# Kernel tuning notes

Hardware: AMD Instinct MI355X
Metric: run time of the kernel (lower is better)

Reference implementation:

```python
import jax, jax.numpy as jnp
import numpy as np


def lstm_encode(x, Wih, Whh, b):
    """x: [S, T, F] -> final hidden state [S, H]. PyTorch LSTM gate order (i, f, g, o)."""
    S = x.shape[0]
    H = Whh.shape[1]

    def step(carry, xt):
        h, c = carry
        z = xt @ Wih.T + h @ Whh.T + b  # [S, 4H]
        i, f, g, o = jnp.split(z, 4, axis=-1)
        c = jax.nn.sigmoid(f) * c + jax.nn.sigmoid(i) * jnp.tanh(g)
        h = jax.nn.sigmoid(o) * jnp.tanh(c)
        return (h, c), None

    init = (jnp.zeros((S, H), x.dtype), jnp.zeros((S, H), x.dtype))
    (h, _), _ = jax.lax.scan(step, init, jnp.swapaxes(x, 0, 1))
    return h


def gatv2(h, Ws, Wd, a, bias):
    """Dense GATv2 on batched fully-connected graphs (no self loops).
    h: [G, N, Hin]; Ws, Wd: [nh, Hin, O]; a: [nh, O]; bias: [nh, O] -> [G, N, nh, O].
    Graph is fully connected (all i != j), so edge-softmax == dense row softmax
    with the diagonal masked out; this is the efficient dense form of the
    gather / LeakyReLU / edge-softmax / scatter pattern in DGL's GATv2Conv."""
    nh = Ws.shape[0]
    N = h.shape[1]
    self_mask = jnp.eye(N, dtype=bool)
    outs = []
    for hd in range(nh):  # small fixed head count; loop caps peak memory
        fs = h @ Ws[hd]  # [G, N, O] source-projected feats (messages)
        fd = h @ Wd[hd]  # [G, N, O] dst-projected feats
        e = jax.nn.leaky_relu(fd[:, :, None, :] + fs[:, None, :, :], 0.2)  # [G, dst, src, O]
        logits = jnp.where(self_mask, -jnp.inf, e @ a[hd])  # [G, dst, src]
        attn = jax.nn.softmax(logits, axis=-1)
        outs.append(jnp.einsum('gds,gso->gdo', attn, fs) + bias[hd])
    return jnp.stack(outs, axis=2)


def cosine(x, y, eps=1e-6):
    xn = x / jnp.maximum(jnp.linalg.norm(x, axis=-1, keepdims=True), eps)
    yn = y / jnp.maximum(jnp.linalg.norm(y, axis=-1, keepdims=True), eps)
    return (xn * yn).sum(-1)


def setup_inputs() -> dict:
    key = jax.random.key(0)
    B, K, T, N, F, H, GH, NH = 16, 4, 64, 128, 16, 32, 32, 8
    ks = jax.random.split(key, 16)

    def rn(k, shape, scale=1.0):
        return jax.random.normal(k, shape, jnp.float32) * scale

    return {
        'anchor': rn(ks[0], (B, T, N, F)),
        'pos': rn(ks[1], (B, T, N, F)),
        'neg': rn(ks[2], (B, K, T, N, F)),
        'hideout': rn(ks[3], (B, 2)),
        'timestep': jax.random.uniform(ks[4], (B, 1), jnp.float32),
        'Wih': rn(ks[5], (4 * H, F), 1.0 / np.sqrt(F)),
        'Whh': rn(ks[6], (4 * H, H), 1.0 / np.sqrt(H)),
        'b_lstm': rn(ks[7], (4 * H,), 0.1),
        'W1s': rn(ks[8], (NH, H, H), 1.0 / np.sqrt(H)),
        'W1d': rn(ks[9], (NH, H, H), 1.0 / np.sqrt(H)),
        'a1': rn(ks[10], (NH, H), 1.0 / np.sqrt(H)),
        'b1': rn(ks[11], (NH, H), 0.1),
        'W2s': rn(ks[12], (1, H, GH), 1.0 / np.sqrt(H)),
        'W2d': rn(ks[13], (1, H, GH), 1.0 / np.sqrt(H)),
        'a2': rn(ks[14], (1, GH), 1.0 / np.sqrt(GH)),
        'b2': rn(ks[15], (1, GH), 0.1),
        'num_agents': 128,
    }


def reference(anchor, pos, neg, hideout, timestep, Wih, Whh, b_lstm,
              W1s, W1d, a1, b1, W2s, W2d, a2, b2, num_agents):
    B, T, N, F = anchor.shape
    K = neg.shape[1]
    H = Whh.shape[1]
    # per-agent time series -> LSTM sequences
    a_seq = jnp.transpose(anchor, (0, 2, 1, 3)).reshape(B * N, T, F)
    p_seq = jnp.transpose(pos, (0, 2, 1, 3)).reshape(B * N, T, F)
    n_seq = jnp.transpose(neg, (0, 1, 3, 2, 4)).reshape(B * K * N, T, F)
    hn = lstm_encode(jnp.concatenate([a_seq, p_seq, n_seq], 0), Wih, Whh, b_lstm)
    hg = hn.reshape(-1, N, H)  # [(2+K)*B, N, H] batched fully-connected graphs
    h1 = gatv2(hg, W1s, W1d, a1, b1).mean(axis=2)  # mean over 8 heads
    h2 = gatv2(h1, W2s, W2d, a2, b2)[:, :, 0, :]   # single head, squeezed
    pooled = h2.mean(axis=1)                        # AvgPooling over nodes
    anchor_res = pooled[:B]
    pos_res = pooled[B:2 * B]
    neg_res = pooled[2 * B:].reshape(B, K, -1)
    sim_pos = cosine(anchor_res, pos_res)[:, None]      # [B, 1]
    sim_neg = cosine(anchor_res[:, None, :], neg_res)   # [B, K]
    all_vecs = jnp.concatenate([sim_neg, sim_pos], axis=1)  # positive last
    contrastive = (-jax.nn.log_softmax(all_vecs, axis=1)[:, -1]).mean()
    res = jnp.concatenate([anchor_res, hideout, timestep], axis=-1)
    return res, contrastive
```

## Files before the change

kernel.cpp:

```cpp
#include <hip/hip_runtime.h>
#include <math.h>


typedef __bf16 bf16x8 __attribute__((ext_vector_type(8)));
typedef float  f32x4  __attribute__((ext_vector_type(4)));
typedef unsigned int u32x4 __attribute__((ext_vector_type(4)));

__device__ __forceinline__ float fast_rcp(float x) { return __builtin_amdgcn_rcpf(x); }
__device__ __forceinline__ float sigm(float x)     { return fast_rcp(1.f + __expf(-x)); }
__device__ __forceinline__ float tanh_fast(float x){ return fmaf(2.f, fast_rcp(1.f + __expf(-2.f * x)), -1.f); }

#define KEEP4(x) asm volatile("" : "+v"(x))

__global__ __launch_bounds__(512, 1) void lstm_mfma_kernel(
    const float* __restrict__ anchor, const float* __restrict__ pos,
    const float* __restrict__ neg, const float* __restrict__ Wih,
    const float* __restrict__ Whh, const float* __restrict__ bias,
    float* __restrict__ hn)
{
    __shared__ float Zl[8 * 320];
    __shared__ unsigned int Hbuf[2][512];
    const int tid  = threadIdx.x;
    const int w    = tid >> 6;
    const int lane = tid & 63;
    const int l15  = lane & 15;
    const int g4   = lane >> 4;
    const int am   = tid >> 5;
    const int aj   = tid & 31;

    #pragma unroll
    for (int i = 0; i < 2; ++i) ((unsigned int*)Hbuf)[tid + i * 512] = 0u;

    const int G = w >> 1, Hh = w & 1;
    const int c = G * 32 + Hh * 16 + l15;
    u32x4 whhH, whhL, wihH;
    {
        union { u32x4 u; bf16x8 v; } th, tl, ti;
        const float* wr = Whh + c * 32 + g4 * 8;
        #pragma unroll
        for (int i = 0; i < 8; ++i) {
            float wv = wr[i];
            __bf16 hi = (__bf16)wv;
            th.v[i] = hi;
            tl.v[i] = (__bf16)(wv - (float)hi);
        }
        if (g4 < 2) {
            const float* wr2 = Wih + c * 16 + g4 * 8;
            #pragma unroll
            for (int i = 0; i < 8; ++i) ti.v[i] = (__bf16)wr2[i];
        } else {
            #pragma unroll
            for (int i = 0; i < 8; ++i) ti.v[i] = (__bf16)0.f;
        }
        whhH = th.u; whhL = tl.u; wihH = ti.u;
    }
    KEEP4(whhH); KEEP4(whhL); KEEP4(wihH);

    const float bi = bias[aj], bf_ = bias[32 + aj], bg = bias[64 + aj], bo = bias[96 + aj];

    const int s = blockIdx.x * 16 + l15;
    const float* xbase; int sl;
    if (s < 2048)      { xbase = anchor; sl = s; }
    else if (s < 4096) { xbase = pos;    sl = s - 2048; }
    else               { xbase = neg;    sl = s - 4096; }
    const bool xact = (g4 < 2);
    const float* xp = xbase + (sl >> 7) * 131072 + (sl & 127) * 16 + (xact ? g4 * 8 : 0);

    const float4 z4 = make_float4(0.f, 0.f, 0.f, 0.f);
    float4 xaA = z4, xbA = z4, xaB = z4, xbB = z4;
    if (xact) {
        xaA = *(const float4*)(xp);        xbA = *(const float4*)(xp + 4);
        xaB = *(const float4*)(xp + 2048); xbB = *(const float4*)(xp + 2052);
    }

    float cstA = 0.f, hA = 0.f;

    const int c0  = g4 * 2;
    const int swz = (l15 & 3) << 1;
    const int ro0 = l15 * 32 + ((c0 ^ swz) << 2);
    const int ro1 = l15 * 32 + (((c0 + 1) ^ swz) << 2);
    const int zw  = w * 320 + l15 * 20 + g4 * 4;
    const int tHh = aj >> 4, jc = (aj & 15) * 20 + am;
    const int zr_i = (0 | tHh) * 320 + jc;
    const int zr_f = (2 | tHh) * 320 + jc;
    const int zr_g = (4 | tHh) * 320 + jc;
    const int zr_o = (6 | tHh) * 320 + jc;
    const int hw   = am * 32 + (((aj >> 2) ^ ((am & 3) << 1)) << 2) + (aj & 3);
    int cur = 0;
    __syncthreads();

    #define LSTM_STEP(XA, XB)                                                          \
    {                                                                                  \
        bf16x8 ax;                                                                     \
        ax[0]=(__bf16)XA.x; ax[1]=(__bf16)XA.y; ax[2]=(__bf16)XA.z; ax[3]=(__bf16)XA.w;\
        ax[4]=(__bf16)XB.x; ax[5]=(__bf16)XB.y; ax[6]=(__bf16)XB.z; ax[7]=(__bf16)XB.w;\
        uint4 v0 = *(const uint4*)(Hbuf[cur] + ro0);                                   \
        uint4 v1 = *(const uint4*)(Hbuf[cur] + ro1);                                   \
        union { unsigned int u[4]; bf16x8 v; } ahi;                                    \
        ahi.u[0] = __builtin_amdgcn_perm(v0.y, v0.x, 0x05040100u);                     \
        ahi.u[1] = __builtin_amdgcn_perm(v0.w, v0.z, 0x05040100u);                     \
        ahi.u[2] = __builtin_amdgcn_perm(v1.y, v1.x, 0x05040100u);                     \
        ahi.u[3] = __builtin_amdgcn_perm(v1.w, v1.z, 0x05040100u);                     \
        f32x4 a = __builtin_amdgcn_mfma_f32_16x16x32_bf16(                             \
            ax, __builtin_bit_cast(bf16x8, wihH), (f32x4)(0.f), 0, 0, 0);              \
        a = __builtin_amdgcn_mfma_f32_16x16x32_bf16(                                   \
            ahi.v, __builtin_bit_cast(bf16x8, whhH), a, 0, 0, 0);                      \
        a = __builtin_amdgcn_mfma_f32_16x16x32_bf16(                                   \
            ahi.v, __builtin_bit_cast(bf16x8, whhL), a, 0, 0, 0);                      \
        *(f32x4*)(Zl + zw) = a;                                                        \
        __syncthreads();                                                               \
        float zi = Zl[zr_i] + bi;                                                      \
        float zf = Zl[zr_f] + bf_;                                                     \
        float zg = Zl[zr_g] + bg;                                                      \
        float zo = Zl[zr_o] + bo;                                                      \
        float cn = fmaf(sigm(zf), cstA, sigm(zi) * tanh_fast(zg));                     \
        cstA = cn;                                                                     \
        hA = sigm(zo) * tanh_fast(cn);                                                 \
        Hbuf[cur ^ 1][hw] = (unsigned int)__builtin_bit_cast(unsigned short,           \
                                                             (__bf16)hA);             \
        __syncthreads();                                                               \
        cur ^= 1;                                                                      \
    }

    for (int t = 0; t < 64; t += 2) {
        float4 cA1 = xaA, cA2 = xbA;
        if (xact && t + 2 < 64) {
            const float* p = xp + (t + 2) * 2048;
            xaA = *(const float4*)(p); xbA = *(const float4*)(p + 4);
        }
        LSTM_STEP(cA1, cA2);

        float4 cB1 = xaB, cB2 = xbB;
        if (xact && t + 3 < 64) {
            const float* p = xp + (t + 3) * 2048;
            xaB = *(const float4*)(p); xbB = *(const float4*)(p + 4);
        }
        LSTM_STEP(cB1, cB2);
    }
    #undef LSTM_STEP

    hn[(blockIdx.x * 16 + am) * 32 + aj] = hA;
}

__device__ __forceinline__ int fsoff(int n) { return n * 36 + ((n >> 5) << 2); }

__global__ __launch_bounds__(256, 2) void gat1_kernel(
    const float* __restrict__ hn, const float* __restrict__ W1s,
    const float* __restrict__ W1d, const float* __restrict__ a1,
    const float* __restrict__ b1, float* __restrict__ h1heads)
{
    const int g = blockIdx.x >> 3, hd = blockIdx.x & 7;
    __shared__ float FSf[128 * 36 + 16];
    __shared__ float FD[128][36];
    __shared__ float AVr[32];
    __shared__ float As06[128];
    __shared__ float Ad06[128];
    const int tid = threadIdx.x;

    if (tid < 32) AVr[tid] = a1[hd * 32 + tid];

    {
        const int o = tid & 31, nb = tid >> 5;
        float wcs[32], wcd[32];
        const float* wsp = W1s + hd * 1024 + o;
        const float* wdp = W1d + hd * 1024 + o;
        #pragma unroll
        for (int k = 0; k < 32; ++k) { wcs[k] = wsp[k * 32]; wcd[k] = wdp[k * 32]; }
        const float* hp = hn + g * 4096 + nb * 512;
        #pragma unroll 1
        for (int n = 0; n < 16; ++n) {
            const int row = nb * 16 + n;
            float a0 = 0.f, a1_ = 0.f, b0 = 0.f, b1_ = 0.f;
            #pragma unroll
            for (int k0 = 0; k0 < 32; k0 += 4) {
                float4 hv = *(const float4*)(hp + n * 32 + k0);
                a0 = fmaf(hv.x, wcs[k0+0], a0); b0 = fmaf(hv.x, wcd[k0+0], b0);
                a1_ = fmaf(hv.y, wcs[k0+1], a1_); b1_ = fmaf(hv.y, wcd[k0+1], b1_);
                a0 = fmaf(hv.z, wcs[k0+2], a0); b0 = fmaf(hv.z, wcd[k0+2], b0);
                a1_ = fmaf(hv.w, wcs[k0+3], a1_); b1_ = fmaf(hv.w, wcd[k0+3], b1_);
            }
            FSf[fsoff(row) + o] = a0 + a1_;
            FD[row][o] = b0 + b1_;
        }
    }
    __syncthreads();

    if (tid < 128) {
        float ss = 0.f, sd = 0.f;
        const float* fr = FSf + fsoff(tid);
        #pragma unroll
        for (int oo = 0; oo < 32; ++oo) {
            int o = (oo + tid) & 31;
            float a = AVr[o];
            ss = fmaf(a, fr[o], ss);
            sd = fmaf(a, FD[tid][o], sd);
        }
        As06[tid] = 0.6f * ss;
        Ad06[tid] = 0.6f * sd;
    }
    __syncthreads();

    const int p = tid >> 2, sq = tid & 3, sbase = sq << 5;
    const int d0 = p, d1 = p + 64;
    float fdr0[32], fdr1[32], avs[32];
    #pragma unroll
    for (int c = 0; c < 8; ++c) {
        float4 v0 = *(const float4*)&FD[d0][c * 4];
        fdr0[c*4+0] = v0.x; fdr0[c*4+1] = v0.y; fdr0[c*4+2] = v0.z; fdr0[c*4+3] = v0.w;
        float4 v1 = *(const float4*)&FD[d1][c * 4];
        fdr1[c*4+0] = v1.x; fdr1[c*4+1] = v1.y; fdr1[c*4+2] = v1.z; fdr1[c*4+3] = v1.w;
        float4 wv = *(const float4*)&AVr[c * 4];
        avs[c*4+0] = 0.4f * wv.x; avs[c*4+1] = 0.4f * wv.y;
        avs[c*4+2] = 0.4f * wv.z; avs[c*4+3] = 0.4f * wv.w;
    }
    const float adc0 = Ad06[d0], adc1 = Ad06[d1];

    float Z0 = 0.f, Z1 = 0.f;
    float acc0[32], acc1[32];
    #pragma unroll
    for (int o = 0; o < 32; ++o) { acc0[o] = 0.f; acc1[o] = 0.f; }
    #pragma unroll 1
    for (int si = 0; si < 32; ++si) {
        const int s = sbase + si;
        const float* fr = FSf + fsoff(s);
        float4 fa[8];
        #pragma unroll
        for (int c = 0; c < 8; ++c) fa[c] = *(const float4*)(fr + c * 4);
        float c00 = 0.f, c01 = 0.f, c02 = 0.f, c03 = 0.f;
        float c10 = 0.f, c11 = 0.f, c12 = 0.f, c13 = 0.f;
        #pragma unroll
        for (int c = 0; c < 8; ++c) {
            float e;
            e = fdr0[c*4+0] + fa[c].x; c00 = fmaf(avs[c*4+0], __builtin_fabsf(e), c00);
            e = fdr1[c*4+0] + fa[c].x; c10 = fmaf(avs[c*4+0], __builtin_fabsf(e), c10);
            e = fdr0[c*4+1] + fa[c].y; c01 = fmaf(avs[c*4+1], __builtin_fabsf(e), c01);
            e = fdr1[c*4+1] + fa[c].y; c11 = fmaf(avs[c*4+1], __builtin_fabsf(e), c11);
            e = fdr0[c*4+2] + fa[c].z; c02 = fmaf(avs[c*4+2], __builtin_fabsf(e), c02);
            e = fdr1[c*4+2] + fa[c].z; c12 = fmaf(avs[c*4+2], __builtin_fabsf(e), c12);
            e = fdr0[c*4+3] + fa[c].w; c03 = fmaf(avs[c*4+3], __builtin_fabsf(e), c03);
            e = fdr1[c*4+3] + fa[c].w; c13 = fmaf(avs[c*4+3], __builtin_fabsf(e), c13);
        }
        const float ass = As06[s];
        float v0 = adc0 + ass + ((c00 + c01) + (c02 + c03));
        float v1 = adc1 + ass + ((c10 + c11) + (c12 + c13));
        float e0 = (s == d0) ? 0.f : __expf(v0);
        float e1 = (s == d1) ? 0.f : __expf(v1);
        Z0 += e0; Z1 += e1;
        #pragma unroll
        for (int c = 0; c < 8; ++c) {
            acc0[c*4+0] = fmaf(e0, fa[c].x, acc0[c*4+0]);
            acc1[c*4+0] = fmaf(e1, fa[c].x, acc1[c*4+0]);
            acc0[c*4+1] = fmaf(e0, fa[c].y, acc0[c*4+1]);
            acc1[c*4+1] = fmaf(e1, fa[c].y, acc1[c*4+1]);
            acc0[c*4+2] = fmaf(e0, fa[c].z, acc0[c*4+2]);
            acc1[c*4+2] = fmaf(e1, fa[c].z, acc1[c*4+2]);
            acc0[c*4+3] = fmaf(e0, fa[c].w, acc0[c*4+3]);
            acc1[c*4+3] = fmaf(e1, fa[c].w, acc1[c*4+3]);
        }
    }
    Z0 += __shfl_xor(Z0, 1); Z0 += __shfl_xor(Z0, 2);
    Z1 += __shfl_xor(Z1, 1); Z1 += __shfl_xor(Z1, 2);
    const float rz0 = fast_rcp(Z0), rz1 = fast_rcp(Z1);
    #pragma unroll
    for (int o = 0; o < 32; ++o) {
        acc0[o] += __shfl_xor(acc0[o], 1);
        acc0[o] += __shfl_xor(acc0[o], 2);
        acc1[o] += __shfl_xor(acc1[o], 1);
        acc1[o] += __shfl_xor(acc1[o], 2);
    }

    if (sq == 0) {
        const float* bp = b1 + hd * 32;
        float* dst0 = h1heads + ((size_t)((g * 8 + hd) * 128 + d0)) * 32;
        float* dst1 = h1heads + ((size_t)((g * 8 + hd) * 128 + d1)) * 32;
        #pragma unroll
        for (int c = 0; c < 8; ++c) {
            float4 v;
            v.x = fmaf(acc0[c*4+0], rz0, bp[c*4+0]);
            v.y = fmaf(acc0[c*4+1], rz0, bp[c*4+1]);
            v.z = fmaf(acc0[c*4+2], rz0, bp[c*4+2]);
            v.w = fmaf(acc0[c*4+3], rz0, bp[c*4+3]);
            *(float4*)(dst0 + c * 4) = v;
            v.x = fmaf(acc1[c*4+0], rz1, bp[c*4+0]);
            v.y = fmaf(acc1[c*4+1], rz1, bp[c*4+1]);
            v.z = fmaf(acc1[c*4+2], rz1, bp[c*4+2]);
            v.w = fmaf(acc1[c*4+3], rz1, bp[c*4+3]);
            *(float4*)(dst1 + c * 4) = v;
        }
    }
}

__global__ __launch_bounds__(256) void gat2_kernel(
    const float* __restrict__ h1heads, const float* __restrict__ W2s,
    const float* __restrict__ W2d, const float* __restrict__ a2,
    const float* __restrict__ b2, float* __restrict__ pooled)
{
    const int g = blockIdx.x;
    __shared__ float HS[128][36];
    __shared__ float FSf[128 * 36 + 16];
    __shared__ float FD[128][36];
    __shared__ float AVr[32];
    __shared__ float As06[128];
    __shared__ float Ad06[128];
    const int tid = threadIdx.x;

    if (tid < 32) AVr[tid] = a2[tid];

    {
        #pragma unroll
        for (int i = 0; i < 4; ++i) {
            int idx4 = i * 256 + tid;
            float sx = 0.f, sy = 0.f, sz = 0.f, sw = 0.f;
            #pragma unroll
            for (int hdd = 0; hdd < 8; ++hdd) {
                const float4* src = (const float4*)(h1heads + (size_t)(g * 8 + hdd) * 4096);
                float4 v = src[idx4];
                sx += v.x; sy += v.y; sz += v.z; sw += v.w;
            }
            int n = idx4 >> 3, k0 = (idx4 & 7) * 4;
            float4 r; r.x = sx * 0.125f; r.y = sy * 0.125f; r.z = sz * 0.125f; r.w = sw * 0.125f;
            *(float4*)&HS[n][k0] = r;
        }
    }
    __syncthreads();

    {
        const int o = tid & 31, nb = tid >> 5;
        float wcs[32], wcd[32];
        const float* wsp = W2s + o;
        const float* wdp = W2d + o;
        #pragma unroll
        for (int k = 0; k < 32; ++k) { wcs[k] = wsp[k * 32]; wcd[k] = wdp[k * 32]; }
        #pragma unroll 1
        for (int n = nb * 16; n < nb * 16 + 16; ++n) {
            float a0 = 0.f, a1_ = 0.f, b0 = 0.f, b1_ = 0.f;
            #pragma unroll
            for (int k0 = 0; k0 < 32; k0 += 4) {
                const float4 hv = *(const float4*)&HS[n][k0];
                a0 = fmaf(hv.x, wcs[k0+0], a0); b0 = fmaf(hv.x, wcd[k0+0], b0);
                a1_ = fmaf(hv.y, wcs[k0+1], a1_); b1_ = fmaf(hv.y, wcd[k0+1], b1_);
                a0 = fmaf(hv.z, wcs[k0+2], a0); b0 = fmaf(hv.z, wcd[k0+2], b0);
                a1_ = fmaf(hv.w, wcs[k0+3], a1_); b1_ = fmaf(hv.w, wcd[k0+3], b1_);
            }
            FSf[fsoff(n) + o] = a0 + a1_;
            FD[n][o] = b0 + b1_;
        }
    }
    __syncthreads();

    if (tid < 128) {
        float ss = 0.f, sd = 0.f;
        const float* fr = FSf + fsoff(tid);
        #pragma unroll
        for (int oo = 0; oo < 32; ++oo) {
            int o = (oo + tid) & 31;
            float a = AVr[o];
            ss = fmaf(a, fr[o], ss);
            sd = fmaf(a, FD[tid][o], sd);
        }
        As06[tid] = 0.6f * ss;
        Ad06[tid] = 0.6f * sd;
    }
    __syncthreads();

    const int d = tid >> 1, sbase = (tid & 1) << 6;
    float fdr[32], avs[32];
    #pragma unroll
    for (int c = 0; c < 8; ++c) {
        float4 v = *(const float4*)&FD[d][c * 4];
        fdr[c*4+0] = v.x; fdr[c*4+1] = v.y; fdr[c*4+2] = v.z; fdr[c*4+3] = v.w;
        float4 wv = *(const float4*)&AVr[c * 4];
        avs[c*4+0] = 0.4f * wv.x; avs[c*4+1] = 0.4f * wv.y;
        avs[c*4+2] = 0.4f * wv.z; avs[c*4+3] = 0.4f * wv.w;
    }
    const float adc = Ad06[d];

    float Z = 0.f;
    float acc[32];
    #pragma unroll
    for (int o = 0; o < 32; ++o) acc[o] = 0.f;
    #pragma unroll 1
    for (int si = 0; si < 64; ++si) {
        const int s = sbase + si;
        const float* fr = FSf + fsoff(s);
        float4 fa[8];
        #pragma unroll
        for (int c = 0; c < 8; ++c) fa[c] = *(const float4*)(fr + c * 4);
        float c0 = 0.f, c1 = 0.f, c2 = 0.f, c3 = 0.f;
        #pragma unroll
        for (int c = 0; c < 8; ++c) {
            float e0 = fdr[c*4+0] + fa[c].x; c0 = fmaf(avs[c*4+0], __builtin_fabsf(e0), c0);
            float e1 = fdr[c*4+1] + fa[c].y; c1 = fmaf(avs[c*4+1], __builtin_fabsf(e1), c1);
            float e2 = fdr[c*4+2] + fa[c].z; c2 = fmaf(avs[c*4+2], __builtin_fabsf(e2), c2);
            float e3 = fdr[c*4+3] + fa[c].w; c3 = fmaf(avs[c*4+3], __builtin_fabsf(e3), c3);
        }
        float v = adc + As06[s] + ((c0 + c1) + (c2 + c3));
        float e = (s == d) ? 0.f : __expf(v);
        Z += e;
        #pragma unroll
        for (int c = 0; c < 8; ++c) {
            acc[c*4+0] = fmaf(e, fa[c].x, acc[c*4+0]);
            acc[c*4+1] = fmaf(e, fa[c].y, acc[c*4+1]);
            acc[c*4+2] = fmaf(e, fa[c].z, acc[c*4+2]);
            acc[c*4+3] = fmaf(e, fa[c].w, acc[c*4+3]);
        }
    }
    Z += __shfl_xor(Z, 1);
    const float rz = fast_rcp(Z);
    #pragma unroll
    for (int o = 0; o < 32; ++o) acc[o] += __shfl_xor(acc[o], 1);

    __syncthreads();
    if ((tid & 1) == 0) {
        #pragma unroll
        for (int c = 0; c < 4; ++c) {
            float4 v;
            v.x = acc[c*4+0] * rz; v.y = acc[c*4+1] * rz;
            v.z = acc[c*4+2] * rz; v.w = acc[c*4+3] * rz;
            *(float4*)&FD[d][c * 4] = v;
        }
    } else {
        #pragma unroll
        for (int c = 4; c < 8; ++c) {
            float4 v;
            v.x = acc[c*4+0] * rz; v.y = acc[c*4+1] * rz;
            v.z = acc[c*4+2] * rz; v.w = acc[c*4+3] * rz;
            *(float4*)&FD[d][c * 4] = v;
        }
    }
    __syncthreads();

    if (tid < 32) {
        float sp = 0.f;
        #pragma unroll 1
        for (int n = 0; n < 128; ++n) sp += FD[n][tid];
        pooled[g * 32 + tid] = fmaf(sp, 1.f / 128.f, b2[tid]);
    }
}

__global__ void final_kernel(const float* __restrict__ pooled,
                             const float* __restrict__ hideout,
                             const float* __restrict__ timestep,
                             float* __restrict__ out)
{
    const int b = threadIdx.x;
    __shared__ float lossArr[16];
    if (b < 16) {
        const float* A  = pooled + b * 32;
        const float* Pv = pooled + (16 + b) * 32;
        float av[32];
        float na = 0.f;
        #pragma unroll
        for (int i = 0; i < 32; ++i) { av[i] = A[i]; na += av[i] * av[i]; }
        float npv = 0.f, dp = 0.f;
        #pragma unroll
        for (int i = 0; i < 32; ++i) { float p = Pv[i]; npv += p * p; dp += av[i] * p; }
        const float eps = 1e-6f;
        const float ia = 1.f / fmaxf(sqrtf(na), eps);
        const float sp = dp * ia / fmaxf(sqrtf(npv), eps);
        float sn[4];
        #pragma unroll
        for (int k = 0; k < 4; ++k) {
            const float* Nv = pooled + (32 + b * 4 + k) * 32;
            float nn = 0.f, dn = 0.f;
            #pragma unroll
            for (int i = 0; i < 32; ++i) { float q = Nv[i]; nn += q * q; dn += av[i] * q; }
            sn[k] = dn * ia / fmaxf(sqrtf(nn), eps);
        }
        float m = sp;
        #pragma unroll
        for (int k = 0; k < 4; ++k) m = fmaxf(m, sn[k]);
        float Z = expf(sp - m);
        #pragma unroll
        for (int k = 0; k < 4; ++k) Z += expf(sn[k] - m);
        lossArr[b] = logf(Z) + m - sp;
        float* r = out + b * 35;
        #pragma unroll
        for (int i = 0; i < 32; ++i) r[i] = av[i];
        r[32] = hideout[b * 2];
        r[33] = hideout[b * 2 + 1];
        r[34] = timestep[b];
    }
    __syncthreads();
    if (b == 0) {
        float s = 0.f;
        #pragma unroll
        for (int i = 0; i < 16; ++i) s += lossArr[i];
        out[560] = s * (1.f / 16.f);
    }
}

extern "C" void kernel_launch(void* const* d_in, const int* in_sizes, int n_in,
                              void* d_out, int out_size, void* d_ws, size_t ws_size,
                              hipStream_t stream) {
    const float* anchor   = (const float*)d_in[0];
    const float* pos      = (const float*)d_in[1];
    const float* neg      = (const float*)d_in[2];
    const float* hideout  = (const float*)d_in[3];
    const float* timestep = (const float*)d_in[4];
    const float* Wih      = (const float*)d_in[5];
    const float* Whh      = (const float*)d_in[6];
    const float* b_lstm   = (const float*)d_in[7];
    const float* W1s      = (const float*)d_in[8];
    const float* W1d      = (const float*)d_in[9];
    const float* a1       = (const float*)d_in[10];
    const float* b1       = (const float*)d_in[11];
    const float* W2s      = (const float*)d_in[12];
    const float* W2d      = (const float*)d_in[13];
    const float* a2       = (const float*)d_in[14];
    const float* b2       = (const float*)d_in[15];
    float* out = (float*)d_out;

    char* ws = (char*)d_ws;
    float* hn      = (float*)(ws);
    float* h1heads = (float*)(ws + 1605632);
    float* pooled  = (float*)(ws + 14188544);

    hipLaunchKernelGGL(lstm_mfma_kernel, dim3(768), dim3(512), 0, stream,
                       anchor, pos, neg, Wih, Whh, b_lstm, hn);
    hipLaunchKernelGGL(gat1_kernel,  dim3(768),  dim3(256), 0, stream,
                       hn, W1s, W1d, a1, b1, h1heads);
    hipLaunchKernelGGL(gat2_kernel,  dim3(96),   dim3(256), 0, stream,
                       h1heads, W2s, W2d, a2, b2, pooled);
    hipLaunchKernelGGL(final_kernel, dim3(1),    dim3(64),  0, stream,
                       pooled, hideout, timestep, out);
}
```

Before: 159.2 us.

## Split LSTM into 8-sequence blocks of 4 waves with two gate tiles each

The LSTM kernel now handles 8 sequences per block using 256 threads instead of 16 sequences with 512 threads, and launches twice as many blocks. Each wave computes two 16-column gate tiles with six MFMAs, and only half the MFMA rows carry real sequences. Smaller blocks make the per-step __syncthreads barriers cheaper and put more independent blocks across the CUs. In exchange, half of the MFMA work is wasted on padded rows, and the Z scratch layout changes to scalar stores.

```diff
diff --git a/kernel.cpp b/kernel.cpp
--- a/kernel.cpp
+++ b/kernel.cpp
@@ -12,13 +12,13 @@
 
 #define KEEP4(x) asm volatile("" : "+v"(x))
 
-__global__ __launch_bounds__(512, 1) void lstm_mfma_kernel(
+__global__ __launch_bounds__(256, 1) void lstm_mfma_kernel(
     const float* __restrict__ anchor, const float* __restrict__ pos,
     const float* __restrict__ neg, const float* __restrict__ Wih,
     const float* __restrict__ Whh, const float* __restrict__ bias,
     float* __restrict__ hn)
 {
-    __shared__ float Zl[8 * 320];
+    __shared__ float Zl[8 * 304];
     __shared__ unsigned int Hbuf[2][512];
     const int tid  = threadIdx.x;
     const int w    = tid >> 6;
@@ -29,12 +29,12 @@
     const int aj   = tid & 31;
 
     #pragma unroll
-    for (int i = 0; i < 2; ++i) ((unsigned int*)Hbuf)[tid + i * 512] = 0u;
-
-    const int G = w >> 1, Hh = w & 1;
-    const int c = G * 32 + Hh * 16 + l15;
-    u32x4 whhH, whhL, wihH;
-    {
+    for (int i = 0; i < 4; ++i) ((unsigned int*)Hbuf)[tid + i * 256] = 0u;
+
+    u32x4 whhH0, whhL0, wihH0, whhH1, whhL1, wihH1;
+    #pragma unroll
+    for (int Hh = 0; Hh < 2; ++Hh) {
+        const int c = w * 32 + Hh * 16 + l15;
         union { u32x4 u; bf16x8 v; } th, tl, ti;
         const float* wr = Whh + c * 32 + g4 * 8;
         #pragma unroll
@@ -52,19 +52,24 @@
             #pragma unroll
             for (int i = 0; i < 8; ++i) ti.v[i] = (__bf16)0.f;
         }
-        whhH = th.u; whhL = tl.u; wihH = ti.u;
-    }
-    KEEP4(whhH); KEEP4(whhL); KEEP4(wihH);
+        if (Hh == 0) { whhH0 = th.u; whhL0 = tl.u; wihH0 = ti.u; }
+        else         { whhH1 = th.u; whhL1 = tl.u; wihH1 = ti.u; }
+    }
+    KEEP4(whhH0); KEEP4(whhL0); KEEP4(wihH0);
+    KEEP4(whhH1); KEEP4(whhL1); KEEP4(wihH1);
 
     const float bi = bias[aj], bf_ = bias[32 + aj], bg = bias[64 + aj], bo = bias[96 + aj];
 
-    const int s = blockIdx.x * 16 + l15;
-    const float* xbase; int sl;
-    if (s < 2048)      { xbase = anchor; sl = s; }
-    else if (s < 4096) { xbase = pos;    sl = s - 2048; }
-    else               { xbase = neg;    sl = s - 4096; }
-    const bool xact = (g4 < 2);
-    const float* xp = xbase + (sl >> 7) * 131072 + (sl & 127) * 16 + (xact ? g4 * 8 : 0);
+    const int s = blockIdx.x * 8 + l15;
+    const bool xact = (g4 < 2) && (l15 < 8);
+    const float* xp = anchor;
+    if (xact) {
+        const float* xbase; int sl;
+        if (s < 2048)      { xbase = anchor; sl = s; }
+        else if (s < 4096) { xbase = pos;    sl = s - 2048; }
+        else               { xbase = neg;    sl = s - 4096; }
+        xp = xbase + (sl >> 7) * 131072 + (sl & 127) * 16 + g4 * 8;
+    }
 
     const float4 z4 = make_float4(0.f, 0.f, 0.f, 0.f);
     float4 xaA = z4, xbA = z4, xaB = z4, xbB = z4;
@@ -79,12 +84,13 @@
     const int swz = (l15 & 3) << 1;
     const int ro0 = l15 * 32 + ((c0 ^ swz) << 2);
     const int ro1 = l15 * 32 + (((c0 + 1) ^ swz) << 2);
-    const int zw  = w * 320 + l15 * 20 + g4 * 4;
-    const int tHh = aj >> 4, jc = (aj & 15) * 20 + am;
-    const int zr_i = (0 | tHh) * 320 + jc;
-    const int zr_f = (2 | tHh) * 320 + jc;
-    const int zr_g = (4 | tHh) * 320 + jc;
-    const int zr_o = (6 | tHh) * 320 + jc;
+    const int zwA = (2 * w) * 304 + (g4 * 4) * 36 + l15;
+    const int zwB = (2 * w + 1) * 304 + (g4 * 4) * 36 + l15;
+    const int tHh = aj >> 4, jc = am * 36 + (aj & 15);
+    const int zr_i = (0 + tHh) * 304 + jc;
+    const int zr_f = (2 + tHh) * 304 + jc;
+    const int zr_g = (4 + tHh) * 304 + jc;
+    const int zr_o = (6 + tHh) * 304 + jc;
     const int hw   = am * 32 + (((aj >> 2) ^ ((am & 3) << 1)) << 2) + (aj & 3);
     int cur = 0;
     __syncthreads();
@@ -101,13 +107,28 @@
         ahi.u[1] = __builtin_amdgcn_perm(v0.w, v0.z, 0x05040100u);                     \
         ahi.u[2] = __builtin_amdgcn_perm(v1.y, v1.x, 0x05040100u);                     \
         ahi.u[3] = __builtin_amdgcn_perm(v1.w, v1.z, 0x05040100u);                     \
-        f32x4 a = __builtin_amdgcn_mfma_f32_16x16x32_bf16(                             \
-            ax, __builtin_bit_cast(bf16x8, wihH), (f32x4)(0.f), 0, 0, 0);              \
-        a = __builtin_amdgcn_mfma_f32_16x16x32_bf16(                                   \
-            ahi.v, __builtin_bit_cast(bf16x8, whhH), a, 0, 0, 0);                      \
-        a = __builtin_amdgcn_mfma_f32_16x16x32_bf16(                                   \
-            ahi.v, __builtin_bit_cast(bf16x8, whhL), a, 0, 0, 0);                      \
-        *(f32x4*)(Zl + zw) = a;                                                        \
+        f32x4 a0 = __builtin_amdgcn_mfma_f32_16x16x32_bf16(                            \
+            ax, __builtin_bit_cast(bf16x8, wihH0), (f32x4)(0.f), 0, 0, 0);             \
+        a0 = __builtin_amdgcn_mfma_f32_16x16x32_bf16(                                  \
+            ahi.v, __builtin_bit_cast(bf16x8, whhH0), a0, 0, 0, 0);                    \
+        a0 = __builtin_amdgcn_mfma_f32_16x16x32_bf16(                                  \
+            ahi.v, __builtin_bit_cast(bf16x8, whhL0), a0, 0, 0, 0);                    \
+        f32x4 a1 = __builtin_amdgcn_mfma_f32_16x16x32_bf16(                            \
+            ax, __builtin_bit_cast(bf16x8, wihH1), (f32x4)(0.f), 0, 0, 0);             \
+        a1 = __builtin_amdgcn_mfma_f32_16x16x32_bf16(                                  \
+            ahi.v, __builtin_bit_cast(bf16x8, whhH1), a1, 0, 0, 0);                    \
+        a1 = __builtin_amdgcn_mfma_f32_16x16x32_bf16(                                  \
+            ahi.v, __builtin_bit_cast(bf16x8, whhL1), a1, 0, 0, 0);                    \
+        if (g4 < 2) {                                                                  \
+            Zl[zwA]       = a0[0];                                                     \
+            Zl[zwA + 36]  = a0[1];                                                     \
+            Zl[zwA + 72]  = a0[2];                                                     \
+            Zl[zwA + 108] = a0[3];                                                     \
+            Zl[zwB]       = a1[0];                                                     \
+            Zl[zwB + 36]  = a1[1];                                                     \
+            Zl[zwB + 72]  = a1[2];                                                     \
+            Zl[zwB + 108] = a1[3];                                                     \
+        }                                                                              \
         __syncthreads();                                                               \
         float zi = Zl[zr_i] + bi;                                                      \
         float zf = Zl[zr_f] + bf_;                                                     \
@@ -139,7 +160,7 @@
     }
     #undef LSTM_STEP
 
-    hn[(blockIdx.x * 16 + am) * 32 + aj] = hA;
+    hn[(blockIdx.x * 8 + am) * 32 + aj] = hA;
 }
 
 __device__ __forceinline__ int fsoff(int n) { return n * 36 + ((n >> 5) << 2); }
@@ -516,7 +537,7 @@
     float* h1heads = (float*)(ws + 1605632);
     float* pooled  = (float*)(ws + 14188544);
 
-    hipLaunchKernelGGL(lstm_mfma_kernel, dim3(768), dim3(512), 0, stream,
+    hipLaunchKernelGGL(lstm_mfma_kernel, dim3(1536), dim3(256), 0, stream,
                        anchor, pos, neg, Wih, Whh, b_lstm, hn);
     hipLaunchKernelGGL(gat1_kernel,  dim3(768),  dim3(256), 0, stream,
                        hn, W1s, W1d, a1, b1, h1heads);
```

Measured after the change: 165.9 us. 4.2% more time.
